# Performance work log

Measured on AMD Instinct MI355X. Metric: run time of the kernel, lower is better.

The kernel has to match this reference:

```python
import jax, jax.numpy as jnp
import numpy as np

N_NODES = 50000
N_EDGES = 300000
NODE_DIM = 11
EDGE_DIM = 5
HID = 256
L = 4
G = 1024  # num graphs
BN_EPS = 1e-5


def setup_inputs() -> dict:
    key = jax.random.key(0)
    ks = jax.random.split(key, 24)
    s = 0.05
    inp = {
        "x": jax.random.normal(ks[0], (N_NODES, NODE_DIM), jnp.float32),
        "edge_index": jax.random.randint(ks[1], (2, N_EDGES), 0, N_NODES, jnp.int32),
        "edge_attr": jax.random.normal(ks[2], (N_EDGES, EDGE_DIM), jnp.float32),
        "batch": jnp.sort(jax.random.randint(ks[3], (N_NODES,), 0, G, jnp.int32)),
        # node encoder
        "enc_W": jax.random.normal(ks[4], (NODE_DIM, HID), jnp.float32) * s,
        "enc_b": jnp.zeros((HID,), jnp.float32),
        # per-layer GINE params (stacked over layers)
        "edge_W": jax.random.normal(ks[5], (L, EDGE_DIM, HID), jnp.float32) * s,
        "edge_b": jnp.zeros((L, HID), jnp.float32),
        "mlp_W1": jax.random.normal(ks[6], (L, HID, HID), jnp.float32) * s,
        "mlp_b1": jnp.zeros((L, HID), jnp.float32),
        "mlp_W2": jax.random.normal(ks[7], (L, HID, HID), jnp.float32) * s,
        "mlp_b2": jnp.zeros((L, HID), jnp.float32),
        "bn_g": jnp.ones((L, HID), jnp.float32),
        "bn_b": jnp.zeros((L, HID), jnp.float32),
        # head: 3*HID -> HID -> HID//2 -> 1
        "head_W1": jax.random.normal(ks[8], (3 * HID, HID), jnp.float32) * s,
        "head_b1": jnp.zeros((HID,), jnp.float32),
        "head_W2": jax.random.normal(ks[9], (HID, HID // 2), jnp.float32) * s,
        "head_b2": jnp.zeros((HID // 2,), jnp.float32),
        "head_W3": jax.random.normal(ks[10], (HID // 2, 1), jnp.float32) * s,
        "head_b3": jnp.zeros((1,), jnp.float32),
    }
    return inp


def _forward(x, edge_attr, enc_W, enc_b, edge_W, edge_b, mlp_W1, mlp_b1,
             mlp_W2, mlp_b2, bn_g, bn_b, head_W1, head_b1, head_W2, head_b2,
             head_W3, head_b3, edge_index, batch):
    n = x.shape[0]
    src, dst = edge_index[0], edge_index[1]  # messages flow src(j) -> dst(i)
    h = jax.nn.relu(x @ enc_W + enc_b)  # [N, HID]
    for l in range(L):
        e = edge_attr @ edge_W[l] + edge_b[l]                 # [E, HID]
        msg = jax.nn.relu(h[src] + e)                         # [E, HID]
        aggr = jax.ops.segment_sum(msg, dst, num_segments=n)  # [N, HID]
        z = h + aggr                                          # (1+eps)*h + aggr, eps=0
        z = jax.nn.relu(z @ mlp_W1[l] + mlp_b1[l]) @ mlp_W2[l] + mlp_b2[l]
        # BatchNorm over node dim (batch statistics)
        mu = jnp.mean(z, axis=0)
        var = jnp.var(z, axis=0)
        z = (z - mu) * jax.lax.rsqrt(var + BN_EPS) * bn_g[l] + bn_b[l]
        h = jax.nn.relu(z) + h  # residual
    # mean / add / max pooling per graph
    sums = jax.ops.segment_sum(h, batch, num_segments=G)      # [G, HID]
    cnt = jax.ops.segment_sum(jnp.ones((n, 1), h.dtype), batch, num_segments=G)
    mean = sums / jnp.maximum(cnt, 1.0)
    mx = jax.ops.segment_max(h, batch, num_segments=G)
    g = jnp.concatenate([mean, sums, mx], axis=1)             # [G, 3*HID]
    g = jax.nn.relu(g @ head_W1 + head_b1)
    g = jax.nn.relu(g @ head_W2 + head_b2)
    out = g @ head_W3 + head_b3
    return out.reshape(-1)  # [G]


def reference(x, edge_index, edge_attr, batch, enc_W, enc_b, edge_W, edge_b,
              mlp_W1, mlp_b1, mlp_W2, mlp_b2, bn_g, bn_b, head_W1, head_b1,
              head_W2, head_b2, head_W3, head_b3):
    return _forward(x, edge_attr, enc_W, enc_b, edge_W, edge_b, mlp_W1, mlp_b1,
                    mlp_W2, mlp_b2, bn_g, bn_b, head_W1, head_b1, head_W2,
                    head_b2, head_W3, head_b3, edge_index, batch)
```

## Files before the change

### kernel.cpp

```cpp
#include <hip/hip_runtime.h>

#define N_NODES 50000
#define N_EDGES 300000
#define G_GRAPHS 1024
#define HID 256
#define NLAYERS 4
#define PAD_SLOTS (N_EDGES + 3 * N_NODES + 64)

typedef unsigned short ushort_t;
typedef __attribute__((ext_vector_type(8))) short bf16x8;
typedef __attribute__((ext_vector_type(8))) unsigned short u16x8;
typedef __attribute__((ext_vector_type(4))) float f32x4;

__device__ __forceinline__ float bf2f(ushort_t u) {
  unsigned int x = ((unsigned int)u) << 16;
  return __builtin_bit_cast(float, x);
}
__device__ __forceinline__ ushort_t f2bf(float f) {
  unsigned int x = __builtin_bit_cast(unsigned int, f);
  unsigned int lsb = (x >> 16) & 1u;
  x += 0x7fffu + lsb;
  return (ushort_t)(x >> 16);
}

__global__ __launch_bounds__(256) void k_encoder(const float* __restrict__ x,
    const float* __restrict__ W, const float* __restrict__ b,
    ushort_t* __restrict__ h, int n)
{
  int j = threadIdx.x;
  float wcol[11];
#pragma unroll
  for (int k = 0; k < 11; ++k) wcol[k] = W[k * HID + j];
  float bj = b[j];
  __shared__ float xs[8][11];
  int base = blockIdx.x * 8;
  if (j < 88) {
    int r = j / 11, k = j % 11;
    int row = base + r;
    if (row < n) xs[r][k] = x[row * 11 + k];
  }
  __syncthreads();
#pragma unroll
  for (int r = 0; r < 8; ++r) {
    int row = base + r;
    if (row >= n) break;
    float acc = bj;
#pragma unroll
    for (int k = 0; k < 11; ++k) acc += xs[r][k] * wcol[k];
    h[(size_t)row * HID + j] = f2bf(fmaxf(acc, 0.f));
  }
}

__global__ __launch_bounds__(256) void k_hist(const int* __restrict__ dst,
    int* __restrict__ offs, int E)
{
  int e = blockIdx.x * 256 + threadIdx.x;
  if (e < E) atomicAdd(&offs[dst[e]], 1);
}

__global__ __launch_bounds__(1024) void k_scanA(int* __restrict__ offs,
    int* __restrict__ btot, int n)
{
  __shared__ int wsum[16];
  int tid = threadIdx.x, lane = tid & 63, wid = tid >> 6;
  int idx = blockIdx.x * 1024 + tid;
  int cnt = (idx < n) ? offs[idx] : 0;
  int v = (cnt + 3) & ~3;
  int x = v;
#pragma unroll
  for (int off = 1; off < 64; off <<= 1) {
    int t = __shfl_up(x, off);
    if (lane >= off) x += t;
  }
  if (lane == 63) wsum[wid] = x;
  __syncthreads();
  if (wid == 0 && lane < 16) {
    int w = wsum[lane];
#pragma unroll
    for (int off = 1; off < 16; off <<= 1) {
      int t = __shfl_up(w, off);
      if (lane >= off) w += t;
    }
    wsum[lane] = w;
  }
  __syncthreads();
  int wbase = (wid == 0) ? 0 : wsum[wid - 1];
  if (idx < n) offs[idx] = wbase + x - v;
  if (tid == 0) btot[blockIdx.x] = wsum[15];
}

__global__ __launch_bounds__(1024) void k_scanC(int* __restrict__ offs,
    int* __restrict__ pstart, const int* __restrict__ btot, int n)
{
  __shared__ int sbase;
  if (threadIdx.x == 0) {
    int s = 0;
    for (int i = 0; i < (int)blockIdx.x; ++i) s += btot[i];
    sbase = s;
    if (blockIdx.x == gridDim.x - 1) pstart[n] = s + btot[blockIdx.x];
  }
  __syncthreads();
  int idx = blockIdx.x * 1024 + threadIdx.x;
  if (idx < n) {
    int v = offs[idx] + sbase;
    offs[idx] = v;
    pstart[idx] = v;
  }
}

__global__ __launch_bounds__(256) void k_fill(const int* __restrict__ src,
    const int* __restrict__ dst, int* __restrict__ offs,
    int* __restrict__ esrc, ushort_t* __restrict__ eab,
    const float* __restrict__ ea, int E)
{
  int e = blockIdx.x * 256 + threadIdx.x;
  if (e < E) {
    int d = dst[e];
    int p = atomicAdd(&offs[d], 1);
    esrc[p] = src[e];
    const float* ep = ea + (size_t)e * 5;
    ushort4 lo = make_ushort4(f2bf(ep[0]), f2bf(ep[1]), f2bf(ep[2]), f2bf(ep[3]));
    ushort4 hi = make_ushort4(f2bf(ep[4]), (ushort_t)0x3f80u, 0, 0);
    *(ushort4*)&eab[(size_t)p * 8] = lo;
    *(ushort4*)&eab[(size_t)p * 8 + 4] = hi;
  }
}

__global__ __launch_bounds__(256) void k_prep(const float* __restrict__ W1,
    const float* __restrict__ W2, ushort_t* __restrict__ Wt1,
    ushort_t* __restrict__ Wt2)
{
  __shared__ float ld[16][257];
  int mat = blockIdx.y & (NLAYERS - 1);
  int which = blockIdx.y >> 2;
  const float* Wm = (which ? W2 : W1) + (size_t)mat * HID * HID;
  ushort_t* Wtm = (which ? Wt2 : Wt1) + (size_t)mat * HID * HID;
  int k0 = blockIdx.x * 16;
  int tid = threadIdx.x;
#pragma unroll
  for (int i = 0; i < 16; ++i) ld[i][tid] = Wm[(size_t)(k0 + i) * HID + tid];
  __syncthreads();
#pragma unroll
  for (int v = 0; v < 4; ++v) {
    ushort4 u = make_ushort4(f2bf(ld[v*4+0][tid]), f2bf(ld[v*4+1][tid]),
                             f2bf(ld[v*4+2][tid]), f2bf(ld[v*4+3][tid]));
    *(ushort4*)&Wtm[(size_t)tid * HID + k0 + v * 4] = u;
  }
}

__global__ __launch_bounds__(256) void k_prept(const float* __restrict__ W,
    ushort_t* __restrict__ Wt, int K, int N)
{
  int idx = blockIdx.x * 256 + threadIdx.x;
  if (idx >= K * N) return;
  int n = idx / K, k = idx % K;
  Wt[idx] = f2bf(W[(size_t)k * N + n]);
}

__device__ __forceinline__ void edge_step(bf16x8 ev, ushort4 hv,
    const float4& w0, const float4& w1, const float4& w2, const float4& w3,
    const float4& w4, const float4& bi,
    float& ax, float& ay, float& az, float& aw)
{
  float v0 = bf2f((ushort_t)ev[0]), v1 = bf2f((ushort_t)ev[1]),
        v2 = bf2f((ushort_t)ev[2]), v3 = bf2f((ushort_t)ev[3]),
        v4 = bf2f((ushort_t)ev[4]), fl = bf2f((ushort_t)ev[5]);
  float m0 = bi.x, m1 = bi.y, m2 = bi.z, m3 = bi.w;
  m0 = fmaf(v0, w0.x, m0); m1 = fmaf(v0, w0.y, m1);
  m2 = fmaf(v0, w0.z, m2); m3 = fmaf(v0, w0.w, m3);
  m0 = fmaf(v1, w1.x, m0); m1 = fmaf(v1, w1.y, m1);
  m2 = fmaf(v1, w1.z, m2); m3 = fmaf(v1, w1.w, m3);
  m0 = fmaf(v2, w2.x, m0); m1 = fmaf(v2, w2.y, m1);
  m2 = fmaf(v2, w2.z, m2); m3 = fmaf(v2, w2.w, m3);
  m0 = fmaf(v3, w3.x, m0); m1 = fmaf(v3, w3.y, m1);
  m2 = fmaf(v3, w3.z, m2); m3 = fmaf(v3, w3.w, m3);
  m0 = fmaf(v4, w4.x, m0); m1 = fmaf(v4, w4.y, m1);
  m2 = fmaf(v4, w4.z, m2); m3 = fmaf(v4, w4.w, m3);
  m0 += bf2f(hv.x); m1 += bf2f(hv.y); m2 += bf2f(hv.z); m3 += bf2f(hv.w);
  ax = fmaf(fl, fmaxf(m0, 0.f), ax);
  ay = fmaf(fl, fmaxf(m1, 0.f), ay);
  az = fmaf(fl, fmaxf(m2, 0.f), az);
  aw = fmaf(fl, fmaxf(m3, 0.f), aw);
}

__global__ __launch_bounds__(256) void k_gather(const ushort_t* __restrict__ h,
    const int* __restrict__ pstart, const int* __restrict__ esrc,
    const ushort_t* __restrict__ eab, const float* __restrict__ eW,
    const float* __restrict__ eb, ushort_t* __restrict__ zin,
    float* __restrict__ stats, int n)
{
  int tid = threadIdx.x;
  if (blockIdx.x == 0) { stats[tid] = 0.f; stats[HID + tid] = 0.f; }
  int wave = tid >> 6, lane = tid & 63;
  int c4 = lane * 4;
  float4 w0 = *(const float4*)&eW[0 * HID + c4];
  float4 w1 = *(const float4*)&eW[1 * HID + c4];
  float4 w2 = *(const float4*)&eW[2 * HID + c4];
  float4 w3 = *(const float4*)&eW[3 * HID + c4];
  float4 w4 = *(const float4*)&eW[4 * HID + c4];
  float4 bi = *(const float4*)&eb[c4];
  int n0 = (blockIdx.x * 4 + wave) * 4;
  if (n0 >= n) return;
  int e0 = __builtin_amdgcn_readfirstlane(pstart[n0]);
  int e1 = __builtin_amdgcn_readfirstlane(pstart[n0 + 1]);
  int e2 = __builtin_amdgcn_readfirstlane(pstart[n0 + 2]);
  int e3 = __builtin_amdgcn_readfirstlane(pstart[n0 + 3]);
  int e4 = __builtin_amdgcn_readfirstlane(pstart[n0 + 4]);
  float A[4][4];
#pragma unroll
  for (int j = 0; j < 4; ++j) {
    ushort4 hv = *(const ushort4*)&h[(size_t)(n0 + j) * HID + c4];
    A[j][0] = bf2f(hv.x); A[j][1] = bf2f(hv.y);
    A[j][2] = bf2f(hv.z); A[j][3] = bf2f(hv.w);
  }
  int p = e0, pend = e4;
  bf16x8 ec0, ec1, ec2, ec3;
  ushort4 hc0, hc1, hc2, hc3;
  int sn0, sn1, sn2, sn3;
  if (p < pend) {
    int sc0 = esrc[p], sc1 = esrc[p + 1], sc2 = esrc[p + 2], sc3 = esrc[p + 3];
    ec0 = *(const bf16x8*)&eab[(size_t)(p + 0) * 8];
    ec1 = *(const bf16x8*)&eab[(size_t)(p + 1) * 8];
    ec2 = *(const bf16x8*)&eab[(size_t)(p + 2) * 8];
    ec3 = *(const bf16x8*)&eab[(size_t)(p + 3) * 8];
    hc0 = *(const ushort4*)&h[(size_t)sc0 * HID + c4];
    hc1 = *(const ushort4*)&h[(size_t)sc1 * HID + c4];
    hc2 = *(const ushort4*)&h[(size_t)sc2 * HID + c4];
    hc3 = *(const ushort4*)&h[(size_t)sc3 * HID + c4];
    int pn = (p + 4 < pend) ? p + 4 : p;
    sn0 = esrc[pn]; sn1 = esrc[pn + 1]; sn2 = esrc[pn + 2]; sn3 = esrc[pn + 3];
  }
  for (; p < pend; p += 4) {
    int pn = (p + 4 < pend) ? p + 4 : p;
    int pnn = (p + 8 < pend) ? p + 8 : p;
    bf16x8 en0 = *(const bf16x8*)&eab[(size_t)(pn + 0) * 8];
    bf16x8 en1 = *(const bf16x8*)&eab[(size_t)(pn + 1) * 8];
    bf16x8 en2 = *(const bf16x8*)&eab[(size_t)(pn + 2) * 8];
    bf16x8 en3 = *(const bf16x8*)&eab[(size_t)(pn + 3) * 8];
    ushort4 hn0 = *(const ushort4*)&h[(size_t)sn0 * HID + c4];
    ushort4 hn1 = *(const ushort4*)&h[(size_t)sn1 * HID + c4];
    ushort4 hn2 = *(const ushort4*)&h[(size_t)sn2 * HID + c4];
    ushort4 hn3 = *(const ushort4*)&h[(size_t)sn3 * HID + c4];
    int sm0 = esrc[pnn], sm1 = esrc[pnn + 1], sm2 = esrc[pnn + 2], sm3 = esrc[pnn + 3];
    float c0 = 0.f, c1 = 0.f, c2 = 0.f, c3 = 0.f;
    edge_step(ec0, hc0, w0, w1, w2, w3, w4, bi, c0, c1, c2, c3);
    edge_step(ec1, hc1, w0, w1, w2, w3, w4, bi, c0, c1, c2, c3);
    edge_step(ec2, hc2, w0, w1, w2, w3, w4, bi, c0, c1, c2, c3);
    edge_step(ec3, hc3, w0, w1, w2, w3, w4, bi, c0, c1, c2, c3);
    if (p < e1)      { A[0][0] += c0; A[0][1] += c1; A[0][2] += c2; A[0][3] += c3; }
    else if (p < e2) { A[1][0] += c0; A[1][1] += c1; A[1][2] += c2; A[1][3] += c3; }
    else if (p < e3) { A[2][0] += c0; A[2][1] += c1; A[2][2] += c2; A[2][3] += c3; }
    else             { A[3][0] += c0; A[3][1] += c1; A[3][2] += c2; A[3][3] += c3; }
    ec0 = en0; ec1 = en1; ec2 = en2; ec3 = en3;
    hc0 = hn0; hc1 = hn1; hc2 = hn2; hc3 = hn3;
    sn0 = sm0; sn1 = sm1; sn2 = sm2; sn3 = sm3;
  }
#pragma unroll
  for (int j = 0; j < 4; ++j) {
    *(ushort4*)&zin[(size_t)(n0 + j) * HID + c4] =
        make_ushort4(f2bf(A[j][0]), f2bf(A[j][1]), f2bf(A[j][2]), f2bf(A[j][3]));
  }
}

__global__ __launch_bounds__(512, 1) void k_mlp(const ushort_t* __restrict__ A,
    const ushort_t* __restrict__ Wt1, const float* __restrict__ b1,
    const ushort_t* __restrict__ Wt2, const float* __restrict__ b2,
    ushort_t* __restrict__ out, float* __restrict__ stats, int M)
{
  __shared__ alignas(16) ushort_t z1s[2][16 * 264];
  int tid = threadIdx.x;
  int wave = tid >> 6, lane = tid & 63;
  int m = lane & 15, quad = lane >> 4;
  int col0 = wave * 32;
  bf16x8 w1f[2][8];
  bf16x8 w2f[2][8];
#pragma unroll
  for (int ct = 0; ct < 2; ++ct)
#pragma unroll
    for (int kt = 0; kt < 8; ++kt) {
      w1f[ct][kt] = *(const bf16x8*)(
          Wt1 + (size_t)(col0 + ct * 16 + m) * HID + kt * 32 + quad * 8);
      w2f[ct][kt] = *(const bf16x8*)(
          Wt2 + (size_t)(col0 + ct * 16 + m) * HID + kt * 32 + quad * 8);
    }
  float bv1[2] = {b1[col0 + m], b1[col0 + 16 + m]};
  float bv2[2] = {b2[col0 + m], b2[col0 + 16 + m]};
  float csum[2] = {0.f, 0.f}, csq[2] = {0.f, 0.f};
  int ntiles = M >> 4;
  int parity = 0;
  int t = blockIdx.x;
  bf16x8 af[8];
  if (t < ntiles) {
    const ushort_t* Ap = A + (size_t)(t * 16 + m) * HID + quad * 8;
#pragma unroll
    for (int kt = 0; kt < 8; ++kt) af[kt] = *(const bf16x8*)(Ap + kt * 32);
  }
  for (; t < ntiles; t += gridDim.x) {
    int tn = t + gridDim.x;
    int tcl = (tn < ntiles) ? tn : t;
    const ushort_t* Apn = A + (size_t)(tcl * 16 + m) * HID + quad * 8;
    bf16x8 afn[8];
#pragma unroll
    for (int kt = 0; kt < 8; ++kt) afn[kt] = *(const bf16x8*)(Apn + kt * 32);
    f32x4 a0 = (f32x4){0.f, 0.f, 0.f, 0.f};
    f32x4 a1 = (f32x4){0.f, 0.f, 0.f, 0.f};
#pragma unroll
    for (int kt = 0; kt < 8; ++kt) {
      a0 = __builtin_amdgcn_mfma_f32_16x16x32_bf16(af[kt], w1f[0][kt], a0, 0, 0, 0);
      a1 = __builtin_amdgcn_mfma_f32_16x16x32_bf16(af[kt], w1f[1][kt], a1, 0, 0, 0);
    }
    ushort_t* buf = z1s[parity];
#pragma unroll
    for (int reg = 0; reg < 4; ++reg) {
      int r = quad * 4 + reg;
      buf[r * 264 + col0 + m]      = f2bf(fmaxf(a0[reg] + bv1[0], 0.f));
      buf[r * 264 + col0 + 16 + m] = f2bf(fmaxf(a1[reg] + bv1[1], 0.f));
    }
    asm volatile("s_waitcnt lgkmcnt(0)" ::: "memory");
    __builtin_amdgcn_s_barrier();
    __builtin_amdgcn_sched_barrier(0);
    f32x4 c0 = (f32x4){0.f, 0.f, 0.f, 0.f};
    f32x4 c1 = (f32x4){0.f, 0.f, 0.f, 0.f};
#pragma unroll
    for (int kt = 0; kt < 8; ++kt) {
      bf16x8 zf = *(const bf16x8*)&buf[m * 264 + kt * 32 + quad * 8];
      c0 = __builtin_amdgcn_mfma_f32_16x16x32_bf16(zf, w2f[0][kt], c0, 0, 0, 0);
      c1 = __builtin_amdgcn_mfma_f32_16x16x32_bf16(zf, w2f[1][kt], c1, 0, 0, 0);
    }
    int rb = t * 16 + quad * 4;
#pragma unroll
    for (int reg = 0; reg < 4; ++reg) {
      float o0 = c0[reg] + bv2[0];
      float o1 = c1[reg] + bv2[1];
      out[(size_t)(rb + reg) * HID + col0 + m] = f2bf(o0);
      out[(size_t)(rb + reg) * HID + col0 + 16 + m] = f2bf(o1);
      csum[0] += o0; csq[0] = fmaf(o0, o0, csq[0]);
      csum[1] += o1; csq[1] = fmaf(o1, o1, csq[1]);
    }
#pragma unroll
    for (int kt = 0; kt < 8; ++kt) af[kt] = afn[kt];
    parity ^= 1;
  }
#pragma unroll
  for (int ct = 0; ct < 2; ++ct) {
    float s = csum[ct], q = csq[ct];
    s += __shfl_xor(s, 16); s += __shfl_xor(s, 32);
    q += __shfl_xor(q, 16); q += __shfl_xor(q, 32);
    if (quad == 0) {
      unsafeAtomicAdd(&stats[col0 + ct * 16 + m], s);
      unsafeAtomicAdd(&stats[HID + col0 + ct * 16 + m], q);
    }
  }
}

__global__ __launch_bounds__(256) void k_bn_apply(const ushort_t* __restrict__ z,
    const float* __restrict__ stats, const float* __restrict__ g,
    const float* __restrict__ b, ushort_t* __restrict__ h, int total4)
{
  int idx = blockIdx.x * 256 + threadIdx.x;
  if (idx >= total4) return;
  int col = (idx & 63) * 4;
  const float inv_n = 1.f / (float)N_NODES;
  float sc[4], sh[4];
#pragma unroll
  for (int c = 0; c < 4; ++c) {
    float mu = stats[col + c] * inv_n;
    float var = stats[HID + col + c] * inv_n - mu * mu;
    float rs = rsqrtf(var + 1e-5f);
    sc[c] = g[col + c] * rs;
    sh[c] = b[col + c] - mu * sc[c];
  }
  ushort4 zv = *(const ushort4*)(z + (size_t)idx * 4);
  ushort4 hv = *(const ushort4*)(h + (size_t)idx * 4);
  float o0 = fmaxf(fmaf(bf2f(zv.x), sc[0], sh[0]), 0.f) + bf2f(hv.x);
  float o1 = fmaxf(fmaf(bf2f(zv.y), sc[1], sh[1]), 0.f) + bf2f(hv.y);
  float o2 = fmaxf(fmaf(bf2f(zv.z), sc[2], sh[2]), 0.f) + bf2f(hv.z);
  float o3 = fmaxf(fmaf(bf2f(zv.w), sc[3], sh[3]), 0.f) + bf2f(hv.w);
  *(ushort4*)(h + (size_t)idx * 4) = make_ushort4(f2bf(o0), f2bf(o1), f2bf(o2), f2bf(o3));
}

__device__ __forceinline__ int lbound(const int* __restrict__ b, int n, int key) {
  int lo = 0, hi = n;
  while (lo < hi) {
    int mid = (lo + hi) >> 1;
    if (b[mid] < key) lo = mid + 1; else hi = mid;
  }
  return lo;
}

__global__ __launch_bounds__(256) void k_pool_bn(const ushort_t* __restrict__ z,
    const float* __restrict__ stats, const float* __restrict__ g_,
    const float* __restrict__ b_, const ushort_t* __restrict__ h,
    const int* __restrict__ batch, ushort_t* __restrict__ gf)
{
  int g = blockIdx.x, j = threadIdx.x;
  const float inv_n = 1.f / (float)N_NODES;
  float mu = stats[j] * inv_n;
  float var = stats[HID + j] * inv_n - mu * mu;
  float rs = rsqrtf(var + 1e-5f);
  float sc = g_[j] * rs;
  float sh = b_[j] - mu * sc;
  int lo = lbound(batch, N_NODES, g);
  int hi = lbound(batch, N_NODES, g + 1);
  float s = 0.f, mx = 0.f;
  for (int i = lo; i < hi; ++i) {
    float zv = bf2f(z[(size_t)i * HID + j]);
    float hv = bf2f(h[(size_t)i * HID + j]);
    float v = fmaxf(fmaf(zv, sc, sh), 0.f) + hv;
    s += v; mx = fmaxf(mx, v);
  }
  float cntv = fmaxf((float)(hi - lo), 1.f);
  size_t base = (size_t)g * 768;
  gf[base + j] = f2bf(s / cntv);
  gf[base + 256 + j] = f2bf(s);
  gf[base + 512 + j] = f2bf(mx);
}

template<int KT, int DO_RELU>
__global__ __launch_bounds__(256, 1) void k_head_gemm(const ushort_t* __restrict__ A,
    const ushort_t* __restrict__ Bt, const float* __restrict__ bias,
    ushort_t* __restrict__ out, int M, int N)
{
  const int K = KT * 32;
  int tid = threadIdx.x;
  int wave = tid >> 6, lane = tid & 63;
  int m = lane & 15, quad = lane >> 4;
  int col = (blockIdx.y * 4 + wave) * 16 + m;
  bf16x8 bfrag[KT];
#pragma unroll
  for (int kt = 0; kt < KT; ++kt)
    bfrag[kt] = *(const bf16x8*)(Bt + (size_t)col * K + kt * 32 + quad * 8);
  float bv = bias[col];
  int ntiles = M >> 4;
  for (int t = blockIdx.x; t < ntiles; t += gridDim.x) {
    const ushort_t* Ap = A + (size_t)(t * 16 + m) * K + quad * 8;
    bf16x8 af[KT];
#pragma unroll
    for (int kt = 0; kt < KT; ++kt) af[kt] = *(const bf16x8*)(Ap + kt * 32);
    f32x4 acc = (f32x4){0.f, 0.f, 0.f, 0.f};
#pragma unroll
    for (int kt = 0; kt < KT; ++kt)
      acc = __builtin_amdgcn_mfma_f32_16x16x32_bf16(af[kt], bfrag[kt], acc, 0, 0, 0);
    int rb = t * 16 + quad * 4;
#pragma unroll
    for (int reg = 0; reg < 4; ++reg) {
      float o = acc[reg] + bv;
      if (DO_RELU) o = fmaxf(o, 0.f);
      out[(size_t)(rb + reg) * N + col] = f2bf(o);
    }
  }
}

__global__ __launch_bounds__(256) void k_head_out(const ushort_t* __restrict__ g2,
    const float* __restrict__ W3, const float* __restrict__ b3,
    float* __restrict__ out)
{
  int wave = threadIdx.x >> 6, lane = threadIdx.x & 63;
  int g = blockIdx.x * 4 + wave;
  ushort2 v = *(const ushort2*)&g2[(size_t)g * 128 + lane * 2];
  float p = bf2f(v.x) * W3[lane * 2] + bf2f(v.y) * W3[lane * 2 + 1];
#pragma unroll
  for (int off = 32; off > 0; off >>= 1) p += __shfl_down(p, off);
  if (lane == 0) out[g] = p + b3[0];
}

extern "C" void kernel_launch(void* const* d_in, const int* in_sizes, int n_in,
                              void* d_out, int out_size, void* d_ws, size_t ws_size,
                              hipStream_t stream)
{
  const float* x     = (const float*)d_in[0];
  const int*   ei    = (const int*)d_in[1];
  const float* ea    = (const float*)d_in[2];
  const int*   batch = (const int*)d_in[3];
  const float* encW  = (const float*)d_in[4];
  const float* encB  = (const float*)d_in[5];
  const float* edgeW = (const float*)d_in[6];
  const float* edgeB = (const float*)d_in[7];
  const float* W1    = (const float*)d_in[8];
  const float* b1    = (const float*)d_in[9];
  const float* W2    = (const float*)d_in[10];
  const float* b2    = (const float*)d_in[11];
  const float* bng   = (const float*)d_in[12];
  const float* bnb   = (const float*)d_in[13];
  const float* hW1   = (const float*)d_in[14];
  const float* hb1   = (const float*)d_in[15];
  const float* hW2   = (const float*)d_in[16];
  const float* hb2   = (const float*)d_in[17];
  const float* hW3   = (const float*)d_in[18];
  const float* hb3   = (const float*)d_in[19];
  float* out = (float*)d_out;

  const size_t NH = (size_t)N_NODES * HID;
  char* base = (char*)d_ws;
  auto alloc = [&](size_t bytes) -> char* {
    char* p = base; base += (bytes + 63) & ~(size_t)63; return p;
  };
  float*    stats = (float*)alloc(512 * 4);
  int*      offs  = (int*)alloc(50001 * 4);
  int*      pstart= (int*)alloc(50001 * 4);
  int*      btot  = (int*)alloc(64 * 4);
  int*      esrc  = (int*)alloc((size_t)PAD_SLOTS * 4);
  ushort_t* eab   = (ushort_t*)alloc((size_t)PAD_SLOTS * 8 * 2);
  ushort_t* Wt1   = (ushort_t*)alloc((size_t)NLAYERS * HID * HID * 2);
  ushort_t* Wt2   = (ushort_t*)alloc((size_t)NLAYERS * HID * HID * 2);
  ushort_t* hW1t  = (ushort_t*)alloc((size_t)768 * 256 * 2);
  ushort_t* hW2t  = (ushort_t*)alloc((size_t)256 * 128 * 2);
  ushort_t* gf    = (ushort_t*)alloc((size_t)G_GRAPHS * 768 * 2);
  ushort_t* g1    = (ushort_t*)alloc((size_t)G_GRAPHS * 256 * 2);
  ushort_t* g2    = (ushort_t*)alloc((size_t)G_GRAPHS * 128 * 2);
  ushort_t* zin   = (ushort_t*)alloc(NH * 2);
  ushort_t* h     = (ushort_t*)alloc(NH * 2);

  const int* src = ei;
  const int* dst = ei + N_EDGES;

  hipMemsetAsync(offs, 0, 50001 * sizeof(int), stream);
  hipMemsetAsync(esrc, 0, (size_t)PAD_SLOTS * 4, stream);
  hipMemsetAsync(eab, 0, (size_t)PAD_SLOTS * 16, stream);
  k_hist<<<(N_EDGES + 255) / 256, 256, 0, stream>>>(dst, offs, N_EDGES);
  const int NSB = (N_NODES + 1023) / 1024;
  k_scanA<<<NSB, 1024, 0, stream>>>(offs, btot, N_NODES);
  k_scanC<<<NSB, 1024, 0, stream>>>(offs, pstart, btot, N_NODES);
  k_fill<<<(N_EDGES + 255) / 256, 256, 0, stream>>>(src, dst, offs, esrc, eab, ea, N_EDGES);
  k_prep<<<dim3(16, 2 * NLAYERS), 256, 0, stream>>>(W1, W2, Wt1, Wt2);
  k_prept<<<(768 * 256 + 255) / 256, 256, 0, stream>>>(hW1, hW1t, 768, 256);
  k_prept<<<(256 * 128 + 255) / 256, 256, 0, stream>>>(hW2, hW2t, 256, 128);

  k_encoder<<<(N_NODES + 7) / 8, 256, 0, stream>>>(x, encW, encB, h, N_NODES);

  for (int l = 0; l < NLAYERS; ++l) {
    k_gather<<<(N_NODES + 15) / 16, 256, 0, stream>>>(
        h, pstart, esrc, eab, edgeW + (size_t)l * 5 * HID, edgeB + (size_t)l * HID,
        zin, stats, N_NODES);
    k_mlp<<<512, 512, 0, stream>>>(
        zin, Wt1 + (size_t)l * HID * HID, b1 + (size_t)l * HID,
        Wt2 + (size_t)l * HID * HID, b2 + (size_t)l * HID, zin, stats, N_NODES);
    if (l < NLAYERS - 1) {
      k_bn_apply<<<(N_NODES * HID / 4 + 255) / 256, 256, 0, stream>>>(
          zin, stats, bng + (size_t)l * HID, bnb + (size_t)l * HID, h,
          N_NODES * HID / 4);
    }
  }

  k_pool_bn<<<G_GRAPHS, 256, 0, stream>>>(
      zin, stats, bng + (size_t)(NLAYERS - 1) * HID,
      bnb + (size_t)(NLAYERS - 1) * HID, h, batch, gf);
  k_head_gemm<24, 1><<<dim3(16, 4), 256, 0, stream>>>(gf, hW1t, hb1, g1, G_GRAPHS, 256);
  k_head_gemm<8, 1><<<dim3(16, 2), 256, 0, stream>>>(g1, hW2t, hb2, g2, G_GRAPHS, 128);
  k_head_out<<<G_GRAPHS / 4, 256, 0, stream>>>(g2, hW3, hb3, out);
}
```

Before: 612.6 us.

## Stage 224-row tiles in LDS and run both MLP GEMMs per block

Replaces the persistent grid-stride MLP kernel, which streamed 16-row tiles with register prefetch and a double-buffered LDS hidden layer. Each block now loads a 224-row slab of the input into LDS in one pass and computes both GEMMs over it, reusing the same LDS buffer for the hidden activations. The grid becomes one block per slab. This is meant to cut per-tile barrier and global-latency overhead and spread weight loads over more rows. In exchange it gives up load/compute overlap inside a block, holds a large accumulator array in registers, and launches roughly one block per CU, which may leave CUs idle.

```diff
diff --git a/kernel.cpp b/kernel.cpp
--- a/kernel.cpp
+++ b/kernel.cpp
@@ -6,6 +6,7 @@
 #define HID 256
 #define NLAYERS 4
 #define PAD_SLOTS (N_EDGES + 3 * N_NODES + 64)
+#define BMT 224
 
 typedef unsigned short ushort_t;
 typedef __attribute__((ext_vector_type(8))) short bf16x8;
@@ -267,88 +268,104 @@
     const ushort_t* __restrict__ Wt2, const float* __restrict__ b2,
     ushort_t* __restrict__ out, float* __restrict__ stats, int M)
 {
-  __shared__ alignas(16) ushort_t z1s[2][16 * 264];
+  __shared__ alignas(16) ushort_t T[BMT][264];
   int tid = threadIdx.x;
   int wave = tid >> 6, lane = tid & 63;
   int m = lane & 15, quad = lane >> 4;
   int col0 = wave * 32;
+  int row0 = blockIdx.x * BMT;
+
+#pragma unroll
+  for (int i = 0; i < 14; ++i) {
+    int flat = i * 512 + tid;
+    int row = flat >> 5, kc = flat & 31;
+    int gr = row0 + row; if (gr > M - 1) gr = M - 1;
+    u16x8 v = *(const u16x8*)(A + (size_t)gr * HID + kc * 8);
+    *(u16x8*)&T[row][kc * 8] = v;
+  }
   bf16x8 w1f[2][8];
-  bf16x8 w2f[2][8];
-#pragma unroll
-  for (int ct = 0; ct < 2; ++ct)
-#pragma unroll
-    for (int kt = 0; kt < 8; ++kt) {
-      w1f[ct][kt] = *(const bf16x8*)(
-          Wt1 + (size_t)(col0 + ct * 16 + m) * HID + kt * 32 + quad * 8);
-      w2f[ct][kt] = *(const bf16x8*)(
-          Wt2 + (size_t)(col0 + ct * 16 + m) * HID + kt * 32 + quad * 8);
-    }
+#pragma unroll
+  for (int nt = 0; nt < 2; ++nt)
+#pragma unroll
+    for (int kt = 0; kt < 8; ++kt)
+      w1f[nt][kt] = *(const bf16x8*)(
+          Wt1 + (size_t)(col0 + nt * 16 + m) * HID + kt * 32 + quad * 8);
   float bv1[2] = {b1[col0 + m], b1[col0 + 16 + m]};
   float bv2[2] = {b2[col0 + m], b2[col0 + 16 + m]};
+  __syncthreads();
+
+  f32x4 acc[14][2];
+#pragma unroll
+  for (int mt = 0; mt < 14; ++mt) {
+    acc[mt][0] = (f32x4){0.f, 0.f, 0.f, 0.f};
+    acc[mt][1] = (f32x4){0.f, 0.f, 0.f, 0.f};
+    bf16x8 af[8];
+#pragma unroll
+    for (int kt = 0; kt < 8; ++kt)
+      af[kt] = *(const bf16x8*)&T[mt * 16 + m][kt * 32 + quad * 8];
+#pragma unroll
+    for (int kt = 0; kt < 8; ++kt) {
+      acc[mt][0] = __builtin_amdgcn_mfma_f32_16x16x32_bf16(af[kt], w1f[0][kt], acc[mt][0], 0, 0, 0);
+      acc[mt][1] = __builtin_amdgcn_mfma_f32_16x16x32_bf16(af[kt], w1f[1][kt], acc[mt][1], 0, 0, 0);
+    }
+  }
+  __syncthreads();
+
+#pragma unroll
+  for (int mt = 0; mt < 14; ++mt)
+#pragma unroll
+    for (int nt = 0; nt < 2; ++nt)
+#pragma unroll
+      for (int reg = 0; reg < 4; ++reg)
+        T[mt * 16 + quad * 4 + reg][col0 + nt * 16 + m] =
+            f2bf(fmaxf(acc[mt][nt][reg] + bv1[nt], 0.f));
+  bf16x8 w2f[2][8];
+#pragma unroll
+  for (int nt = 0; nt < 2; ++nt)
+#pragma unroll
+    for (int kt = 0; kt < 8; ++kt)
+      w2f[nt][kt] = *(const bf16x8*)(
+          Wt2 + (size_t)(col0 + nt * 16 + m) * HID + kt * 32 + quad * 8);
+  __syncthreads();
+
+#pragma unroll
+  for (int mt = 0; mt < 14; ++mt) {
+    acc[mt][0] = (f32x4){0.f, 0.f, 0.f, 0.f};
+    acc[mt][1] = (f32x4){0.f, 0.f, 0.f, 0.f};
+    bf16x8 af[8];
+#pragma unroll
+    for (int kt = 0; kt < 8; ++kt)
+      af[kt] = *(const bf16x8*)&T[mt * 16 + m][kt * 32 + quad * 8];
+#pragma unroll
+    for (int kt = 0; kt < 8; ++kt) {
+      acc[mt][0] = __builtin_amdgcn_mfma_f32_16x16x32_bf16(af[kt], w2f[0][kt], acc[mt][0], 0, 0, 0);
+      acc[mt][1] = __builtin_amdgcn_mfma_f32_16x16x32_bf16(af[kt], w2f[1][kt], acc[mt][1], 0, 0, 0);
+    }
+  }
+
   float csum[2] = {0.f, 0.f}, csq[2] = {0.f, 0.f};
-  int ntiles = M >> 4;
-  int parity = 0;
-  int t = blockIdx.x;
-  bf16x8 af[8];
-  if (t < ntiles) {
-    const ushort_t* Ap = A + (size_t)(t * 16 + m) * HID + quad * 8;
-#pragma unroll
-    for (int kt = 0; kt < 8; ++kt) af[kt] = *(const bf16x8*)(Ap + kt * 32);
-  }
-  for (; t < ntiles; t += gridDim.x) {
-    int tn = t + gridDim.x;
-    int tcl = (tn < ntiles) ? tn : t;
-    const ushort_t* Apn = A + (size_t)(tcl * 16 + m) * HID + quad * 8;
-    bf16x8 afn[8];
-#pragma unroll
-    for (int kt = 0; kt < 8; ++kt) afn[kt] = *(const bf16x8*)(Apn + kt * 32);
-    f32x4 a0 = (f32x4){0.f, 0.f, 0.f, 0.f};
-    f32x4 a1 = (f32x4){0.f, 0.f, 0.f, 0.f};
-#pragma unroll
-    for (int kt = 0; kt < 8; ++kt) {
-      a0 = __builtin_amdgcn_mfma_f32_16x16x32_bf16(af[kt], w1f[0][kt], a0, 0, 0, 0);
-      a1 = __builtin_amdgcn_mfma_f32_16x16x32_bf16(af[kt], w1f[1][kt], a1, 0, 0, 0);
-    }
-    ushort_t* buf = z1s[parity];
-#pragma unroll
-    for (int reg = 0; reg < 4; ++reg) {
-      int r = quad * 4 + reg;
-      buf[r * 264 + col0 + m]      = f2bf(fmaxf(a0[reg] + bv1[0], 0.f));
-      buf[r * 264 + col0 + 16 + m] = f2bf(fmaxf(a1[reg] + bv1[1], 0.f));
-    }
-    asm volatile("s_waitcnt lgkmcnt(0)" ::: "memory");
-    __builtin_amdgcn_s_barrier();
-    __builtin_amdgcn_sched_barrier(0);
-    f32x4 c0 = (f32x4){0.f, 0.f, 0.f, 0.f};
-    f32x4 c1 = (f32x4){0.f, 0.f, 0.f, 0.f};
-#pragma unroll
-    for (int kt = 0; kt < 8; ++kt) {
-      bf16x8 zf = *(const bf16x8*)&buf[m * 264 + kt * 32 + quad * 8];
-      c0 = __builtin_amdgcn_mfma_f32_16x16x32_bf16(zf, w2f[0][kt], c0, 0, 0, 0);
-      c1 = __builtin_amdgcn_mfma_f32_16x16x32_bf16(zf, w2f[1][kt], c1, 0, 0, 0);
-    }
-    int rb = t * 16 + quad * 4;
-#pragma unroll
-    for (int reg = 0; reg < 4; ++reg) {
-      float o0 = c0[reg] + bv2[0];
-      float o1 = c1[reg] + bv2[1];
-      out[(size_t)(rb + reg) * HID + col0 + m] = f2bf(o0);
-      out[(size_t)(rb + reg) * HID + col0 + 16 + m] = f2bf(o1);
-      csum[0] += o0; csq[0] = fmaf(o0, o0, csq[0]);
-      csum[1] += o1; csq[1] = fmaf(o1, o1, csq[1]);
-    }
-#pragma unroll
-    for (int kt = 0; kt < 8; ++kt) af[kt] = afn[kt];
-    parity ^= 1;
-  }
-#pragma unroll
-  for (int ct = 0; ct < 2; ++ct) {
-    float s = csum[ct], q = csq[ct];
+#pragma unroll
+  for (int mt = 0; mt < 14; ++mt) {
+    if (row0 + mt * 16 < M) {
+#pragma unroll
+      for (int nt = 0; nt < 2; ++nt) {
+#pragma unroll
+        for (int reg = 0; reg < 4; ++reg) {
+          float o = acc[mt][nt][reg] + bv2[nt];
+          out[(size_t)(row0 + mt * 16 + quad * 4 + reg) * HID + col0 + nt * 16 + m] = f2bf(o);
+          csum[nt] += o; csq[nt] = fmaf(o, o, csq[nt]);
+        }
+      }
+    }
+  }
+#pragma unroll
+  for (int nt = 0; nt < 2; ++nt) {
+    float s = csum[nt], q = csq[nt];
     s += __shfl_xor(s, 16); s += __shfl_xor(s, 32);
     q += __shfl_xor(q, 16); q += __shfl_xor(q, 32);
     if (quad == 0) {
-      unsafeAtomicAdd(&stats[col0 + ct * 16 + m], s);
-      unsafeAtomicAdd(&stats[HID + col0 + ct * 16 + m], q);
+      unsafeAtomicAdd(&stats[col0 + nt * 16 + m], s);
+      unsafeAtomicAdd(&stats[HID + col0 + nt * 16 + m], q);
     }
   }
 }
@@ -528,11 +545,13 @@
 
   k_encoder<<<(N_NODES + 7) / 8, 256, 0, stream>>>(x, encW, encB, h, N_NODES);
 
+  const int NB_MLP = (N_NODES + BMT - 1) / BMT;
+
   for (int l = 0; l < NLAYERS; ++l) {
     k_gather<<<(N_NODES + 15) / 16, 256, 0, stream>>>(
         h, pstart, esrc, eab, edgeW + (size_t)l * 5 * HID, edgeB + (size_t)l * HID,
         zin, stats, N_NODES);
-    k_mlp<<<512, 512, 0, stream>>>(
+    k_mlp<<<NB_MLP, 512, 0, stream>>>(
         zin, Wt1 + (size_t)l * HID * HID, b1 + (size_t)l * HID,
         Wt2 + (size_t)l * HID * HID, b2 + (size_t)l * HID, zin, stats, N_NODES);
     if (l < NLAYERS - 1) {
```

Result: faster. 530.5 us (-13.4%).
